# Kernel optimization log

Measured on AMD Instinct MI355X. Metric: run time of the kernel, lower is better.

Reference implementation:

```python
import jax, jax.numpy as jnp
import numpy as np
import math

B, S, D, H, L, DF = 16, 512, 512, 8, 6, 2048
DK = D // H
EPS = 1e-6


def _xavier(key, shape):
    # xavier_uniform over the last two dims (matches nn.init.xavier_uniform_)
    fan_in, fan_out = shape[-2], shape[-1]
    lim = math.sqrt(6.0 / (fan_in + fan_out))
    return jax.random.uniform(key, shape, jnp.float32, -lim, lim)


def setup_inputs() -> dict:
    key = jax.random.key(0)
    ks = jax.random.split(key, 12)
    return {
        "x": jax.random.normal(ks[0], (B, S, D), jnp.float32),
        "pe_table": jax.random.normal(ks[1], (S, D), jnp.float32),  # _4by8_pe weight
        "pe_q_w": _xavier(ks[2], (D, D)), "pe_q_b": jnp.zeros((D,), jnp.float32),
        "pe_k_w": _xavier(ks[3], (D, D)), "pe_k_b": jnp.zeros((D,), jnp.float32),
        "Wq": _xavier(ks[4], (L, D, D)), "bq": jnp.zeros((L, D), jnp.float32),
        "Wk": _xavier(ks[5], (L, D, D)), "bk": jnp.zeros((L, D), jnp.float32),
        "Wv": _xavier(ks[6], (L, D, D)), "bv": jnp.zeros((L, D), jnp.float32),
        "Wo": _xavier(ks[7], (L, D, D)), "bo": jnp.zeros((L, D), jnp.float32),
        "ln1_g": jnp.ones((L, D), jnp.float32), "ln1_b": jnp.zeros((L, D), jnp.float32),
        "W1": _xavier(ks[8], (L, D, DF)), "b1": jnp.zeros((L, DF), jnp.float32),
        "W2": _xavier(ks[9], (L, DF, D)), "b2": jnp.zeros((L, D), jnp.float32),
        "ln2_g": jnp.ones((L, D), jnp.float32), "ln2_b": jnp.zeros((L, D), jnp.float32),
    }


def _layernorm(y, g, b):
    m = jnp.mean(y, axis=-1, keepdims=True)
    v = jnp.var(y, axis=-1, keepdims=True)  # biased, as torch LayerNorm
    return (y - m) * jax.lax.rsqrt(v + EPS) * g + b


def reference(x, pe_table, pe_q_w, pe_q_b, pe_k_w, pe_k_b,
              Wq, bq, Wk, bk, Wv, bv, Wo, bo,
              ln1_g, ln1_b, W1, b1, W2, b2, ln2_g, ln2_b):
    scale = math.sqrt(2 * DK)
    h = x * math.sqrt(D)

    # scores_pe is identical for every batch element (pe_onehot = arange repeated)
    pq = (pe_table @ pe_q_w + pe_q_b).reshape(S, H, DK).transpose(1, 0, 2)  # [H,S,dk]
    pk = (pe_table @ pe_k_w + pe_k_b).reshape(S, H, DK).transpose(1, 0, 2)  # [H,S,dk]
    scores_pe = jnp.einsum('hqd,hkd->hqk', pq, pk) / scale  # [H,S,S]

    def step(h, p):
        wq, bq_, wk, bk_, wv, bv_, wo, bo_, g1, gb1, w1, fb1, w2, fb2, g2, gb2 = p
        q = (h @ wq + bq_).reshape(B, S, H, DK).transpose(0, 2, 1, 3)  # [B,H,S,dk]
        k = (h @ wk + bk_).reshape(B, S, H, DK).transpose(0, 2, 1, 3)
        v = (h @ wv + bv_).reshape(B, S, H, DK).transpose(0, 2, 1, 3)
        scores = jnp.einsum('bhqd,bhkd->bhqk', q, k) / scale + scores_pe  # [B,H,S,S]
        attn = jax.nn.softmax(scores, axis=-1)
        o = jnp.einsum('bhqk,bhkd->bhqd', attn, v).transpose(0, 2, 1, 3).reshape(B, S, D)
        o = o @ wo + bo_
        h1 = _layernorm(o + h, g1, gb1)
        f = jax.nn.gelu(h1 @ w1 + fb1, approximate=False) @ w2 + fb2
        h2 = _layernorm(f + h1, g2, gb2)
        return h2, None

    params = (Wq, bq, Wk, bk, Wv, bv, Wo, bo, ln1_g, ln1_b, W1, b1, W2, b2, ln2_g, ln2_b)
    h, _ = jax.lax.scan(step, h, params)
    pe_out = jnp.broadcast_to(pe_table, (B, S, D))
    return h, pe_out
```

## Files before the change

### kernel.cpp

```cpp
#include <hip/hip_runtime.h>
#include <hip/hip_bf16.h>

typedef __hip_bfloat16 bf16;
typedef short bf16x8 __attribute__((ext_vector_type(8)));
typedef float f32x4 __attribute__((ext_vector_type(4)));

#define DEV static __device__ __forceinline__

DEV f32x4 fzero4(){ f32x4 z; z[0]=0.f; z[1]=0.f; z[2]=0.f; z[3]=0.f; return z; }

DEV void gl2lds16(const bf16* g, bf16* l){
  __builtin_amdgcn_global_load_lds(
    (const __attribute__((address_space(1))) void*)g,
    (__attribute__((address_space(3))) void*)l, 16, 0, 0);
}

enum { EP_F32=0, EP_BF16=1, EP_GELU=2, EP_HILO=3, EP_QKV=4 };

template<int EPI, int NMT>
__global__ __launch_bounds__(256) void gemm_bt(
    const bf16* A0, const bf16* A1, const bf16* A2,
    const bf16* B0, const bf16* B1, const bf16* B2,
    int npass, int lda, int ldb, int M, int N, int K,
    const float* __restrict__ bs0, const float* __restrict__ bs1, const float* __restrict__ bs2,
    float alpha, void* o0, void* o1, void* o2,
    int nn, int mchunk, int azs, int bzs, int ozs)
{
  constexpr int BM = NMT*32;
  __shared__ __align__(16) bf16 As[2][BM*32];
  __shared__ __align__(16) bf16 Bs[2][128*32];
  const int t = threadIdx.x;
  const int lane = t & 63;
  const int w = t >> 6;
  const int wr = w >> 1, wc = w & 1;
  const int bid = blockIdx.x;
  const int xcd = bid & 7;
  const int idx = bid >> 3;
  const int qm = idx / nn;
  const int mb = xcd*mchunk + qm;
  const int nb = idx - qm*nn;
  const int m0 = mb*BM, n0 = nb*128;
  const int l15 = lane & 15, l4 = lane >> 4;
  const int grow = (lane >> 2);
  const int gcol = (lane & 3) * 8;
  const int z = blockIdx.z;
  if (azs){ A0 += (size_t)z*azs; if(A1) A1 += (size_t)z*azs; if(A2) A2 += (size_t)z*azs; }
  if (bzs){ B0 += (size_t)z*bzs; if(B1) B1 += (size_t)z*bzs; if(B2) B2 += (size_t)z*bzs; }

  auto Aof = [&](int p){ return (p==0)?A0:((p==1)?A1:A2); };
  auto Bof = [&](int p){ return (p==0)?B0:((p==1)?B1:B2); };

  auto stageAB = [&](int cb, const bf16* Ag, const bf16* Bg, int k0){
    if constexpr (NMT==4){
      #pragma unroll
      for (int q=0;q<2;q++){
        int row = w*32 + q*16 + grow;
        gl2lds16(Ag + (size_t)(m0+row)*lda + k0 + gcol, As[cb] + (w*32+q*16)*32);
        gl2lds16(Bg + (size_t)(n0+row)*ldb + k0 + gcol, Bs[cb] + (w*32+q*16)*32);
      }
    } else {
      int rA = w*16 + grow;
      gl2lds16(Ag + (size_t)(m0+rA)*lda + k0 + gcol, As[cb] + w*16*32);
      #pragma unroll
      for (int sb=0;sb<2;sb++){
        int rB = (2*w+sb)*16 + grow;
        gl2lds16(Bg + (size_t)(n0+rB)*ldb + k0 + gcol, Bs[cb] + (2*w+sb)*16*32);
      }
    }
  };

  f32x4 acc[NMT][4];
  #pragma unroll
  for (int i=0;i<NMT;i++)
    #pragma unroll
    for (int j=0;j<4;j++) acc[i][j] = fzero4();

  int cur = 0;
  stageAB(0, A0, B0, 0);
  for (int p=0;p<npass;p++){
    for (int k0=0;k0<K;k0+=32){
      __syncthreads();
      int kn = k0 + 32;
      if (kn < K)            stageAB(cur^1, Aof(p), Bof(p), kn);
      else if (p+1 < npass)  stageAB(cur^1, Aof(p+1), Bof(p+1), 0);
      bf16x8 af[NMT], bfv[4];
      #pragma unroll
      for (int mt=0;mt<NMT;mt++) af[mt] = *(const bf16x8*)(As[cur] + (wr*(NMT*16)+mt*16+l15)*32 + 8*l4);
      #pragma unroll
      for (int nt=0;nt<4;nt++) bfv[nt] = *(const bf16x8*)(Bs[cur] + (wc*64+nt*16+l15)*32 + 8*l4);
      #pragma unroll
      for (int mt=0;mt<NMT;mt++)
        #pragma unroll
        for (int nt=0;nt<4;nt++)
          acc[mt][nt] = __builtin_amdgcn_mfma_f32_16x16x32_bf16(af[mt], bfv[nt], acc[mt][nt], 0, 0, 0);
      cur ^= 1;
    }
  }

  #pragma unroll
  for (int mt=0;mt<NMT;mt++){
    #pragma unroll
    for (int nt=0;nt<4;nt++){
      const int crow = m0 + wr*(NMT*16) + mt*16 + l4*4;
      const int ccol = n0 + wc*64 + nt*16 + l15;
      #pragma unroll
      for (int j=0;j<4;j++){
        float v = acc[mt][nt][j];
        int r = crow + j;
        if (EPI==EP_F32){
          float b = bs0 ? bs0[ccol] : 0.f;
          ((float*)o0)[(size_t)r*N + ccol] = alpha*v + b;
        } else if (EPI==EP_BF16){
          float b = bs0 ? bs0[ccol] : 0.f;
          ((bf16*)o0 + (size_t)z*ozs)[(size_t)r*N + ccol] = __float2bfloat16(alpha*v + b);
        } else if (EPI==EP_GELU){
          float xx = v + bs0[ccol];
          float g = 0.5f*xx*(1.f + erff(xx*0.70710678118654752f));
          ((bf16*)o0)[(size_t)r*N + ccol] = __float2bfloat16(g);
        } else if (EPI==EP_HILO){
          float xx = v + bs0[ccol];
          bf16 hi = __float2bfloat16(xx);
          ((bf16*)o0)[(size_t)r*N + ccol] = hi;
          ((bf16*)o1)[(size_t)r*N + ccol] = __float2bfloat16(xx - __bfloat162float(hi));
        } else {
          int n = ccol;
          if (n < 512){
            ((bf16*)o0)[(size_t)r*512 + n] = __float2bfloat16(v + bs0[n]);
          } else if (n < 1024){
            ((bf16*)o1)[(size_t)r*512 + (n-512)] = __float2bfloat16(v + bs1[n-512]);
          } else {
            int d = n - 1024;
            int bb = r >> 9, s = r & 511;
            int hh = d >> 6, dd = d & 63;
            ((bf16*)o2)[(size_t)(((bb*8)+hh)*64 + dd)*512 + s] = __float2bfloat16(v + bs2[d]);
          }
        }
      }
    }
  }
}

template<int SPLIT>
__global__ __launch_bounds__(256) void attn_mfma(
  const bf16* __restrict__ Q, const bf16* __restrict__ Qlo,
  const bf16* __restrict__ Kh, const bf16* __restrict__ Klo,
  const bf16* __restrict__ VT, const bf16* __restrict__ SPE,
  bf16* __restrict__ O)
{
  __shared__ __align__(16) bf16 K_lds[64*64];
  __shared__ __align__(16) bf16 V_lds[64*64];
  __shared__ __align__(16) bf16 Klo_lds[SPLIT ? 64*64 : 8];
  __shared__ __align__(16) bf16 P_lds[4][16*64];
  const int t = threadIdx.x;
  const int lane = t & 63, w = t >> 6;
  const int l15 = lane & 15, l4 = lane >> 4;
  const int bid = blockIdx.x;
  const int h = bid & 7;
  const int s2 = bid >> 3;
  const int b = s2 >> 3, qblk = s2 & 7;
  const int q0 = qblk*64 + w*16;
  const float inv_scale = 0.08838834764831845f;
  const int xorv = (l15 & 7) << 3;

  bf16x8 qf[2], qflo[2];
  #pragma unroll
  for (int kst=0;kst<2;kst++){
    qf[kst] = *(const bf16x8*)(Q + (size_t)(b*512 + q0 + l15)*512 + h*64 + kst*32 + 8*l4);
    if (SPLIT) qflo[kst] = *(const bf16x8*)(Qlo + (size_t)(b*512 + q0 + l15)*512 + h*64 + kst*32 + 8*l4);
  }
  f32x4 accO[4];
  #pragma unroll
  for (int dt=0;dt<4;dt++) accO[dt] = fzero4();
  float mrow[4], lrow[4];
  #pragma unroll
  for (int j=0;j<4;j++){ mrow[j] = -1e30f; lrow[j] = 0.f; }

  const bf16* spe_h = SPE + (size_t)h*262144;
  const bf16* vbase = VT + (size_t)((b*8)+h)*32768;

  for (int n0=0;n0<512;n0+=64){
    #pragma unroll
    for (int st=0;st<2;st++){
      int rl = w*16 + st*8 + (lane>>3);
      int jj = (lane&7) ^ (rl&7);
      gl2lds16(Kh + (size_t)(b*512 + n0 + rl)*512 + h*64 + jj*8, K_lds + (w*16+st*8)*64);
      if (SPLIT)
        gl2lds16(Klo + (size_t)(b*512 + n0 + rl)*512 + h*64 + jj*8, Klo_lds + (w*16+st*8)*64);
      gl2lds16(vbase + (size_t)rl*512 + n0 + jj*8, V_lds + (w*16+st*8)*64);
    }
    __syncthreads();

    f32x4 sc[4];
    #pragma unroll
    for (int c=0;c<4;c++) sc[c] = fzero4();
    __builtin_amdgcn_s_setprio(1);
    #pragma unroll
    for (int c=0;c<4;c++){
      const int rr = c*16 + l15;
      #pragma unroll
      for (int kst=0;kst<2;kst++){
        bf16x8 kf = *(const bf16x8*)(K_lds + rr*64 + ((kst*32 + 8*l4) ^ xorv));
        sc[c] = __builtin_amdgcn_mfma_f32_16x16x32_bf16(qf[kst], kf, sc[c], 0,0,0);
        if (SPLIT){
          sc[c] = __builtin_amdgcn_mfma_f32_16x16x32_bf16(qflo[kst], kf, sc[c], 0,0,0);
          bf16x8 kfl = *(const bf16x8*)(Klo_lds + rr*64 + ((kst*32 + 8*l4) ^ xorv));
          sc[c] = __builtin_amdgcn_mfma_f32_16x16x32_bf16(qf[kst], kfl, sc[c], 0,0,0);
        }
      }
    }
    __builtin_amdgcn_s_setprio(0);
    float sv[4][4];
    #pragma unroll
    for (int c=0;c<4;c++)
      #pragma unroll
      for (int j=0;j<4;j++){
        int qr = q0 + l4*4 + j;
        sv[c][j] = sc[c][j]*inv_scale + __bfloat162float(spe_h[(size_t)qr*512 + n0 + c*16 + l15]);
      }
    float mx[4];
    float dm = -1e30f;
    #pragma unroll
    for (int j=0;j<4;j++){
      mx[j] = fmaxf(fmaxf(sv[0][j],sv[1][j]), fmaxf(sv[2][j],sv[3][j]));
      dm = fmaxf(dm, mx[j] - mrow[j]);
    }
    if (__any(dm > 8.f)){
      #pragma unroll
      for (int j=0;j<4;j++){
        float m2 = mx[j];
        m2 = fmaxf(m2, __shfl_xor(m2,1));
        m2 = fmaxf(m2, __shfl_xor(m2,2));
        m2 = fmaxf(m2, __shfl_xor(m2,4));
        m2 = fmaxf(m2, __shfl_xor(m2,8));
        float mn = fmaxf(mrow[j], m2);
        float fac = __expf(mrow[j] - mn);
        mrow[j] = mn;
        lrow[j] *= fac;
        #pragma unroll
        for (int dt=0;dt<4;dt++) accO[dt][j] *= fac;
      }
    }
    #pragma unroll
    for (int j=0;j<4;j++){
      int row = l4*4 + j;
      float ts = 0.f;
      #pragma unroll
      for (int c=0;c<4;c++){
        float pv = __expf(sv[c][j] - mrow[j]);
        ts += pv;
        P_lds[w][row*64 + ((c*16 + l15) ^ ((row&7)<<3))] = __float2bfloat16(pv);
      }
      ts += __shfl_xor(ts,1); ts += __shfl_xor(ts,2);
      ts += __shfl_xor(ts,4); ts += __shfl_xor(ts,8);
      lrow[j] += ts;
    }
    __builtin_amdgcn_s_setprio(1);
    #pragma unroll
    for (int kv=0;kv<2;kv++){
      bf16x8 pf = *(const bf16x8*)(P_lds[w] + l15*64 + ((kv*32 + 8*l4) ^ xorv));
      #pragma unroll
      for (int dt=0;dt<4;dt++){
        const int d = dt*16 + l15;
        bf16x8 vf = *(const bf16x8*)(V_lds + d*64 + ((kv*32 + 8*l4) ^ xorv));
        accO[dt] = __builtin_amdgcn_mfma_f32_16x16x32_bf16(pf, vf, accO[dt], 0,0,0);
      }
    }
    __builtin_amdgcn_s_setprio(0);
    __syncthreads();
  }
  #pragma unroll
  for (int dt=0;dt<4;dt++)
    #pragma unroll
    for (int j=0;j<4;j++){
      float v = accO[dt][j] / lrow[j];
      int r = q0 + l4*4 + j;
      O[(size_t)(b*512+r)*512 + h*64 + dt*16 + l15] = __float2bfloat16(v);
    }
}

__global__ __launch_bounds__(256) void ln_kernel(
  const float* __restrict__ tmp, const float* __restrict__ resid,
  const float* __restrict__ g, const float* __restrict__ bta,
  float* __restrict__ outf, bf16* __restrict__ outb)
{
  const int row = blockIdx.x*4 + (threadIdx.x>>6);
  const int lane = threadIdx.x & 63;
  const size_t base = (size_t)row*512 + lane*8;
  float4 a0 = *(const float4*)(tmp+base),   a1 = *(const float4*)(tmp+base+4);
  float4 r0 = *(const float4*)(resid+base), r1 = *(const float4*)(resid+base+4);
  float x[8];
  x[0]=a0.x+r0.x; x[1]=a0.y+r0.y; x[2]=a0.z+r0.z; x[3]=a0.w+r0.w;
  x[4]=a1.x+r1.x; x[5]=a1.y+r1.y; x[6]=a1.z+r1.z; x[7]=a1.w+r1.w;
  float s=0.f, sq=0.f;
  #pragma unroll
  for (int i=0;i<8;i++){ s += x[i]; sq += x[i]*x[i]; }
  #pragma unroll
  for (int d=1; d<64; d<<=1){ s += __shfl_xor(s,d); sq += __shfl_xor(sq,d); }
  float mean = s*(1.f/512.f);
  float var = sq*(1.f/512.f) - mean*mean;
  float rr = rsqrtf(var + 1e-6f);
  #pragma unroll
  for (int i=0;i<8;i++){
    int d = lane*8 + i;
    float y = (x[i]-mean)*rr*g[d] + bta[d];
    outf[base+i] = y;
    outb[base+i] = __float2bfloat16(y);
  }
}

template<bool LO>
__global__ __launch_bounds__(256) void tcast(
  const float* __restrict__ src, int srcStride,
  bf16* __restrict__ dst, int dstStride, bf16* __restrict__ dlo,
  int R, int C)
{
  __shared__ float tile[32][33];
  const int z = blockIdx.z;
  src += (size_t)z*srcStride;
  dst += (size_t)z*dstStride;
  const int tx = threadIdx.x & 31, ty = threadIdx.x >> 5;
  const int r0 = blockIdx.y*32, c0 = blockIdx.x*32;
  #pragma unroll
  for (int p=0;p<4;p++)
    tile[ty+8*p][tx] = src[(size_t)(r0+ty+8*p)*C + c0+tx];
  __syncthreads();
  #pragma unroll
  for (int p=0;p<4;p++){
    float v = tile[tx][ty+8*p];
    bf16 hi = __float2bfloat16(v);
    dst[(size_t)(c0+ty+8*p)*R + r0+tx] = hi;
    if (LO) dlo[(size_t)(c0+ty+8*p)*R + r0+tx] = __float2bfloat16(v - __bfloat162float(hi));
  }
}

__global__ void castbf(const float* __restrict__ in, bf16* __restrict__ out, int n){
  int i = blockIdx.x*blockDim.x + threadIdx.x;
  if (i < n) out[i] = __float2bfloat16(in[i]);
}

__global__ void init_h(const float* __restrict__ x, float* __restrict__ hf,
                       bf16* __restrict__ hb, bf16* __restrict__ hlo, int n){
  int i = blockIdx.x*blockDim.x + threadIdx.x;
  if (i < n){
    float v = x[i]*22.627416997969522f;
    hf[i] = v;
    bf16 hi = __float2bfloat16(v);
    hb[i] = hi;
    hlo[i] = __float2bfloat16(v - __bfloat162float(hi));
  }
}

__global__ void write_out(const float* __restrict__ hf, const float* __restrict__ pe,
                          float* __restrict__ out, int n1){
  int i = blockIdx.x*blockDim.x + threadIdx.x;
  if (i < n1){
    out[i] = hf[i];
    out[n1 + i] = pe[i & 262143];
  }
}

extern "C" void kernel_launch(void* const* d_in, const int* in_sizes, int n_in,
                              void* d_out, int out_size, void* d_ws, size_t ws_size,
                              hipStream_t stream)
{
  const float* x    = (const float*)d_in[0];
  const float* pe   = (const float*)d_in[1];
  const float* peqw = (const float*)d_in[2];
  const float* peqb = (const float*)d_in[3];
  const float* pekw = (const float*)d_in[4];
  const float* pekb = (const float*)d_in[5];
  const float* Wq   = (const float*)d_in[6];
  const float* bq   = (const float*)d_in[7];
  const float* Wk   = (const float*)d_in[8];
  const float* bk   = (const float*)d_in[9];
  const float* Wv   = (const float*)d_in[10];
  const float* bv   = (const float*)d_in[11];
  const float* Wo   = (const float*)d_in[12];
  const float* bo   = (const float*)d_in[13];
  const float* g1   = (const float*)d_in[14];
  const float* bb1  = (const float*)d_in[15];
  const float* W1   = (const float*)d_in[16];
  const float* fb1  = (const float*)d_in[17];
  const float* W2   = (const float*)d_in[18];
  const float* fb2  = (const float*)d_in[19];
  const float* g2   = (const float*)d_in[20];
  const float* bb2  = (const float*)d_in[21];

  char* wp = (char*)d_ws;
  auto carve = [&](size_t bytes)->void*{ void* r = (void*)wp; wp += (bytes + 255) & ~(size_t)255; return r; };
  float* hf   = (float*)carve(16777216);
  float* h1f  = (float*)carve(16777216);
  char*  regB = (char*)carve(16777216);
  float* tmp  = (float*)regB;
  bf16*  qlo  = (bf16*)regB;
  bf16*  klo  = (bf16*)(regB + 8388608);
  bf16* hb    = (bf16*)carve(8388608);
  bf16* hlo   = (bf16*)carve(8388608);
  bf16* h1b   = (bf16*)carve(8388608);
  char* regA  = (char*)carve(33554432);
  bf16* gbuf  = (bf16*)regA;
  bf16* qb    = (bf16*)regA;
  bf16* kbuf  = (bf16*)(regA + 8388608);
  bf16* vT    = (bf16*)(regA + 16777216);
  bf16* obuf  = (bf16*)(regA + 25165824);
  bf16* WqkvT = (bf16*)carve(9437184);
  bf16* WoT   = (bf16*)carve(3145728);
  bf16* W1T   = (bf16*)carve(12582912);
  bf16* W2T   = (bf16*)carve(12582912);
  bf16* Wq0h  = (bf16*)carve(524288);
  bf16* Wq0l  = (bf16*)carve(524288);
  bf16* Wk0h  = (bf16*)carve(524288);
  bf16* Wk0l  = (bf16*)carve(524288);
  bf16* peb   = (bf16*)carve(524288);
  bf16* pqwT  = (bf16*)carve(524288);
  bf16* pkwT  = (bf16*)carve(524288);
  bf16* pqb   = (bf16*)carve(524288);
  bf16* pkb   = (bf16*)carve(524288);
  bf16* spe   = (bf16*)carve(4194304);

  dim3 B256(256);
  const float INV_SCALE = 0.08838834764831845f;

  tcast<false><<<dim3(16,16,6),B256,0,stream>>>(Wq, 262144, WqkvT,          786432, nullptr, 512, 512);
  tcast<false><<<dim3(16,16,6),B256,0,stream>>>(Wk, 262144, WqkvT + 262144, 786432, nullptr, 512, 512);
  tcast<false><<<dim3(16,16,6),B256,0,stream>>>(Wv, 262144, WqkvT + 524288, 786432, nullptr, 512, 512);
  tcast<false><<<dim3(16,16,6),B256,0,stream>>>(Wo, 262144, WoT, 262144, nullptr, 512, 512);
  tcast<false><<<dim3(64,16,6),B256,0,stream>>>(W1, 1048576, W1T, 1048576, nullptr, 512, 2048);
  tcast<false><<<dim3(16,64,6),B256,0,stream>>>(W2, 1048576, W2T, 1048576, nullptr, 2048, 512);
  tcast<false><<<dim3(16,16,1),B256,0,stream>>>(peqw, 262144, pqwT, 262144, nullptr, 512, 512);
  tcast<false><<<dim3(16,16,1),B256,0,stream>>>(pekw, 262144, pkwT, 262144, nullptr, 512, 512);
  tcast<true ><<<dim3(16,16,1),B256,0,stream>>>(Wq, 262144, Wq0h, 262144, Wq0l, 512, 512);
  tcast<true ><<<dim3(16,16,1),B256,0,stream>>>(Wk, 262144, Wk0h, 262144, Wk0l, 512, 512);
  castbf<<<1024,B256,0,stream>>>(pe, peb, 262144);
  init_h<<<16384,B256,0,stream>>>(x, hf, hb, hlo, 4194304);

  gemm_bt<EP_BF16,2><<<dim3(32),B256,0,stream>>>(peb,nullptr,nullptr, pqwT,nullptr,nullptr, 1, 512,512, 512,512,512, peqb,nullptr,nullptr, 1.f, pqb,nullptr,nullptr, 4,1, 0,0,0);
  gemm_bt<EP_BF16,2><<<dim3(32),B256,0,stream>>>(peb,nullptr,nullptr, pkwT,nullptr,nullptr, 1, 512,512, 512,512,512, pekb,nullptr,nullptr, 1.f, pkb,nullptr,nullptr, 4,1, 0,0,0);
  gemm_bt<EP_BF16,2><<<dim3(32,1,8),B256,0,stream>>>(pqb,nullptr,nullptr, pkb,nullptr,nullptr, 1, 512,512, 512,512,64, nullptr,nullptr,nullptr, INV_SCALE, spe,nullptr,nullptr, 4,1, 64,64,262144);

  for (int l=0;l<6;l++){
    const bf16* WQKV = WqkvT + l*786432;
    const float* bql = bq + l*512;
    const float* bkl = bk + l*512;
    const float* bvl = bv + l*512;
    gemm_bt<EP_QKV,4><<<dim3(768),B256,0,stream>>>(hb,nullptr,nullptr, WQKV,nullptr,nullptr, 1, 512,512, 8192,1536,512, bql,bkl,bvl, 1.f, qb, kbuf, vT, 12,8, 0,0,0);
    if (l==0){
      gemm_bt<EP_HILO,2><<<dim3(512),B256,0,stream>>>(hb,hb,hlo, Wq0h,Wq0l,Wq0h, 3, 512,512, 8192,512,512, bql,nullptr,nullptr, 1.f, qb, qlo, nullptr, 4,16, 0,0,0);
      gemm_bt<EP_HILO,2><<<dim3(512),B256,0,stream>>>(hb,hb,hlo, Wk0h,Wk0l,Wk0h, 3, 512,512, 8192,512,512, bkl,nullptr,nullptr, 1.f, kbuf, klo, nullptr, 4,16, 0,0,0);
      attn_mfma<1><<<dim3(1024),B256,0,stream>>>(qb,qlo,kbuf,klo,vT,spe,obuf);
    } else {
      attn_mfma<0><<<dim3(1024),B256,0,stream>>>(qb,qb,kbuf,kbuf,vT,spe,obuf);
    }
    gemm_bt<EP_F32,2><<<dim3(512),B256,0,stream>>>(obuf,nullptr,nullptr, WoT+l*262144,nullptr,nullptr, 1, 512,512, 8192,512,512, bo+l*512,nullptr,nullptr, 1.f, tmp,nullptr,nullptr, 4,16, 0,0,0);
    ln_kernel<<<2048,B256,0,stream>>>(tmp, hf, g1+l*512, bb1+l*512, h1f, h1b);
    gemm_bt<EP_GELU,4><<<dim3(1024),B256,0,stream>>>(h1b,nullptr,nullptr, W1T+l*1048576,nullptr,nullptr, 1, 512,512, 8192,2048,512, fb1+l*2048,nullptr,nullptr, 1.f, gbuf,nullptr,nullptr, 16,8, 0,0,0);
    gemm_bt<EP_F32,2><<<dim3(512),B256,0,stream>>>(gbuf,nullptr,nullptr, W2T+l*1048576,nullptr,nullptr, 1, 2048,2048, 8192,512,2048, fb2+l*512,nullptr,nullptr, 1.f, tmp,nullptr,nullptr, 4,16, 0,0,0);
    ln_kernel<<<2048,B256,0,stream>>>(tmp, h1f, g2+l*512, bb2+l*512, hf, hb);
  }
  write_out<<<16384,B256,0,stream>>>(hf, pe, (float*)d_out, 4194304);
}
```

Baseline: 1.304 ms.

## Double-buffer attention K/V, fold softmax scale into Q, bf16 GEMM-LN intermediates

The attention kernel now double-buffers K/V tiles in LDS (non-split path), so the next tile's global-to-LDS load overlaps the current tile's compute. It also preloads the positional score bias as the MFMA accumulator init. The softmax scale and log2(e) are folded into Q and the PE scores so exp2f replaces __expf and the per-element scale multiply goes away. The rescale threshold is loosened from 8 to 12. The Wo and W2 GEMM outputs feeding LayerNorm are stored as bf16 instead of f32, halving that traffic at some accuracy cost, and a bit-shift bf16-to-float helper is added.

```diff
diff --git a/kernel.cpp b/kernel.cpp
--- a/kernel.cpp
+++ b/kernel.cpp
@@ -8,6 +8,15 @@
 #define DEV static __device__ __forceinline__
 
 DEV f32x4 fzero4(){ f32x4 z; z[0]=0.f; z[1]=0.f; z[2]=0.f; z[3]=0.f; return z; }
+
+DEV float bf2f(bf16 v){
+  unsigned int u = ((unsigned int)*(unsigned short*)&v) << 16;
+  return *(float*)&u;
+}
+DEV float bf2s(short s){
+  unsigned int u = ((unsigned int)(unsigned short)s) << 16;
+  return *(float*)&u;
+}
 
 DEV void gl2lds16(const bf16* g, bf16* l){
   __builtin_amdgcn_global_load_lds(
@@ -118,14 +127,14 @@
           float g = 0.5f*xx*(1.f + erff(xx*0.70710678118654752f));
           ((bf16*)o0)[(size_t)r*N + ccol] = __float2bfloat16(g);
         } else if (EPI==EP_HILO){
-          float xx = v + bs0[ccol];
+          float xx = (v + bs0[ccol]) * alpha;
           bf16 hi = __float2bfloat16(xx);
           ((bf16*)o0)[(size_t)r*N + ccol] = hi;
-          ((bf16*)o1)[(size_t)r*N + ccol] = __float2bfloat16(xx - __bfloat162float(hi));
+          ((bf16*)o1)[(size_t)r*N + ccol] = __float2bfloat16(xx - bf2f(hi));
         } else {
           int n = ccol;
           if (n < 512){
-            ((bf16*)o0)[(size_t)r*512 + n] = __float2bfloat16(v + bs0[n]);
+            ((bf16*)o0)[(size_t)r*512 + n] = __float2bfloat16((v + bs0[n]) * alpha);
           } else if (n < 1024){
             ((bf16*)o1)[(size_t)r*512 + (n-512)] = __float2bfloat16(v + bs1[n-512]);
           } else {
@@ -147,8 +156,9 @@
   const bf16* __restrict__ VT, const bf16* __restrict__ SPE,
   bf16* __restrict__ O)
 {
-  __shared__ __align__(16) bf16 K_lds[64*64];
-  __shared__ __align__(16) bf16 V_lds[64*64];
+  constexpr int NB = SPLIT ? 1 : 2;
+  __shared__ __align__(16) bf16 K_lds[NB][64*64];
+  __shared__ __align__(16) bf16 V_lds[NB][64*64];
   __shared__ __align__(16) bf16 Klo_lds[SPLIT ? 64*64 : 8];
   __shared__ __align__(16) bf16 P_lds[4][16*64];
   const int t = threadIdx.x;
@@ -159,8 +169,22 @@
   const int s2 = bid >> 3;
   const int b = s2 >> 3, qblk = s2 & 7;
   const int q0 = qblk*64 + w*16;
-  const float inv_scale = 0.08838834764831845f;
   const int xorv = (l15 & 7) << 3;
+
+  const bf16* spe_h = SPE + (size_t)h*262144;
+  const bf16* vbase = VT + (size_t)((b*8)+h)*32768;
+
+  auto stageKV = [&](int cb, int n0){
+    #pragma unroll
+    for (int st=0;st<2;st++){
+      int rl = w*16 + st*8 + (lane>>3);
+      int jj = (lane&7) ^ (rl&7);
+      gl2lds16(Kh + (size_t)(b*512 + n0 + rl)*512 + h*64 + jj*8, K_lds[cb] + (w*16+st*8)*64);
+      if (SPLIT)
+        gl2lds16(Klo + (size_t)(b*512 + n0 + rl)*512 + h*64 + jj*8, Klo_lds + (w*16+st*8)*64);
+      gl2lds16(vbase + (size_t)rl*512 + n0 + jj*8, V_lds[cb] + (w*16+st*8)*64);
+    }
+  };
 
   bf16x8 qf[2], qflo[2];
   #pragma unroll
@@ -175,31 +199,24 @@
   #pragma unroll
   for (int j=0;j<4;j++){ mrow[j] = -1e30f; lrow[j] = 0.f; }
 
-  const bf16* spe_h = SPE + (size_t)h*262144;
-  const bf16* vbase = VT + (size_t)((b*8)+h)*32768;
-
-  for (int n0=0;n0<512;n0+=64){
-    #pragma unroll
-    for (int st=0;st<2;st++){
-      int rl = w*16 + st*8 + (lane>>3);
-      int jj = (lane&7) ^ (rl&7);
-      gl2lds16(Kh + (size_t)(b*512 + n0 + rl)*512 + h*64 + jj*8, K_lds + (w*16+st*8)*64);
-      if (SPLIT)
-        gl2lds16(Klo + (size_t)(b*512 + n0 + rl)*512 + h*64 + jj*8, Klo_lds + (w*16+st*8)*64);
-      gl2lds16(vbase + (size_t)rl*512 + n0 + jj*8, V_lds + (w*16+st*8)*64);
-    }
+  int cur = 0;
+  stageKV(0, 0);
+  for (int it=0; it<8; ++it){
+    const int n0 = it*64;
+    f32x4 sc[4];
+    #pragma unroll
+    for (int c=0;c<4;c++)
+      #pragma unroll
+      for (int j=0;j<4;j++)
+        sc[c][j] = bf2f(spe_h[(size_t)(q0 + l4*4 + j)*512 + n0 + c*16 + l15]);
     __syncthreads();
-
-    f32x4 sc[4];
-    #pragma unroll
-    for (int c=0;c<4;c++) sc[c] = fzero4();
-    __builtin_amdgcn_s_setprio(1);
+    if (NB==2 && it+1 < 8) stageKV(cur^1, n0+64);
     #pragma unroll
     for (int c=0;c<4;c++){
       const int rr = c*16 + l15;
       #pragma unroll
       for (int kst=0;kst<2;kst++){
-        bf16x8 kf = *(const bf16x8*)(K_lds + rr*64 + ((kst*32 + 8*l4) ^ xorv));
+        bf16x8 kf = *(const bf16x8*)(K_lds[cur] + rr*64 + ((kst*32 + 8*l4) ^ xorv));
         sc[c] = __builtin_amdgcn_mfma_f32_16x16x32_bf16(qf[kst], kf, sc[c], 0,0,0);
         if (SPLIT){
           sc[c] = __builtin_amdgcn_mfma_f32_16x16x32_bf16(qflo[kst], kf, sc[c], 0,0,0);
@@ -208,23 +225,14 @@
         }
       }
     }
-    __builtin_amdgcn_s_setprio(0);
-    float sv[4][4];
-    #pragma unroll
-    for (int c=0;c<4;c++)
-      #pragma unroll
-      for (int j=0;j<4;j++){
-        int qr = q0 + l4*4 + j;
-        sv[c][j] = sc[c][j]*inv_scale + __bfloat162float(spe_h[(size_t)qr*512 + n0 + c*16 + l15]);
-      }
     float mx[4];
     float dm = -1e30f;
     #pragma unroll
     for (int j=0;j<4;j++){
-      mx[j] = fmaxf(fmaxf(sv[0][j],sv[1][j]), fmaxf(sv[2][j],sv[3][j]));
+      mx[j] = fmaxf(fmaxf(sc[0][j],sc[1][j]), fmaxf(sc[2][j],sc[3][j]));
       dm = fmaxf(dm, mx[j] - mrow[j]);
     }
-    if (__any(dm > 8.f)){
+    if (__any(dm > 12.f)){
       #pragma unroll
       for (int j=0;j<4;j++){
         float m2 = mx[j];
@@ -233,7 +241,7 @@
         m2 = fmaxf(m2, __shfl_xor(m2,4));
         m2 = fmaxf(m2, __shfl_xor(m2,8));
         float mn = fmaxf(mrow[j], m2);
-        float fac = __expf(mrow[j] - mn);
+        float fac = exp2f(mrow[j] - mn);
         mrow[j] = mn;
         lrow[j] *= fac;
         #pragma unroll
@@ -246,7 +254,7 @@
       float ts = 0.f;
       #pragma unroll
       for (int c=0;c<4;c++){
-        float pv = __expf(sv[c][j] - mrow[j]);
+        float pv = exp2f(sc[c][j] - mrow[j]);
         ts += pv;
         P_lds[w][row*64 + ((c*16 + l15) ^ ((row&7)<<3))] = __float2bfloat16(pv);
       }
@@ -254,19 +262,21 @@
       ts += __shfl_xor(ts,4); ts += __shfl_xor(ts,8);
       lrow[j] += ts;
     }
-    __builtin_amdgcn_s_setprio(1);
     #pragma unroll
     for (int kv=0;kv<2;kv++){
       bf16x8 pf = *(const bf16x8*)(P_lds[w] + l15*64 + ((kv*32 + 8*l4) ^ xorv));
       #pragma unroll
       for (int dt=0;dt<4;dt++){
         const int d = dt*16 + l15;
-        bf16x8 vf = *(const bf16x8*)(V_lds + d*64 + ((kv*32 + 8*l4) ^ xorv));
+        bf16x8 vf = *(const bf16x8*)(V_lds[cur] + d*64 + ((kv*32 + 8*l4) ^ xorv));
         accO[dt] = __builtin_amdgcn_mfma_f32_16x16x32_bf16(pf, vf, accO[dt], 0,0,0);
       }
     }
-    __builtin_amdgcn_s_setprio(0);
-    __syncthreads();
+    if (NB==1){
+      __syncthreads();
+      if (it+1 < 8) stageKV(0, n0+64);
+    }
+    cur ^= (NB-1);
   }
   #pragma unroll
   for (int dt=0;dt<4;dt++)
@@ -279,18 +289,20 @@
 }
 
 __global__ __launch_bounds__(256) void ln_kernel(
-  const float* __restrict__ tmp, const float* __restrict__ resid,
+  const bf16* __restrict__ tmp, const float* __restrict__ resid,
   const float* __restrict__ g, const float* __restrict__ bta,
   float* __restrict__ outf, bf16* __restrict__ outb)
 {
   const int row = blockIdx.x*4 + (threadIdx.x>>6);
   const int lane = threadIdx.x & 63;
   const size_t base = (size_t)row*512 + lane*8;
-  float4 a0 = *(const float4*)(tmp+base),   a1 = *(const float4*)(tmp+base+4);
+  bf16x8 a = *(const bf16x8*)(tmp+base);
   float4 r0 = *(const float4*)(resid+base), r1 = *(const float4*)(resid+base+4);
   float x[8];
-  x[0]=a0.x+r0.x; x[1]=a0.y+r0.y; x[2]=a0.z+r0.z; x[3]=a0.w+r0.w;
-  x[4]=a1.x+r1.x; x[5]=a1.y+r1.y; x[6]=a1.z+r1.z; x[7]=a1.w+r1.w;
+  x[0]=bf2s(a[0])+r0.x; x[1]=bf2s(a[1])+r0.y;
+  x[2]=bf2s(a[2])+r0.z; x[3]=bf2s(a[3])+r0.w;
+  x[4]=bf2s(a[4])+r1.x; x[5]=bf2s(a[5])+r1.y;
+  x[6]=bf2s(a[6])+r1.z; x[7]=bf2s(a[7])+r1.w;
   float s=0.f, sq=0.f;
   #pragma unroll
   for (int i=0;i<8;i++){ s += x[i]; sq += x[i]*x[i]; }
@@ -329,7 +341,7 @@
     float v = tile[tx][ty+8*p];
     bf16 hi = __float2bfloat16(v);
     dst[(size_t)(c0+ty+8*p)*R + r0+tx] = hi;
-    if (LO) dlo[(size_t)(c0+ty+8*p)*R + r0+tx] = __float2bfloat16(v - __bfloat162float(hi));
+    if (LO) dlo[(size_t)(c0+ty+8*p)*R + r0+tx] = __float2bfloat16(v - bf2f(hi));
   }
 }
 
@@ -346,7 +358,7 @@
     hf[i] = v;
     bf16 hi = __float2bfloat16(v);
     hb[i] = hi;
-    hlo[i] = __float2bfloat16(v - __bfloat162float(hi));
+    hlo[i] = __float2bfloat16(v - bf2f(hi));
   }
 }
 
@@ -391,7 +403,7 @@
   float* hf   = (float*)carve(16777216);
   float* h1f  = (float*)carve(16777216);
   char*  regB = (char*)carve(16777216);
-  float* tmp  = (float*)regB;
+  bf16*  tmpb = (bf16*)regB;
   bf16*  qlo  = (bf16*)regB;
   bf16*  klo  = (bf16*)(regB + 8388608);
   bf16* hb    = (bf16*)carve(8388608);
@@ -419,7 +431,7 @@
   bf16* spe   = (bf16*)carve(4194304);
 
   dim3 B256(256);
-  const float INV_SCALE = 0.08838834764831845f;
+  const float QSCALE = 0.08838834764831845f * 1.4426950408889634f;
 
   tcast<false><<<dim3(16,16,6),B256,0,stream>>>(Wq, 262144, WqkvT,          786432, nullptr, 512, 512);
   tcast<false><<<dim3(16,16,6),B256,0,stream>>>(Wk, 262144, WqkvT + 262144, 786432, nullptr, 512, 512);
@@ -436,26 +448,26 @@
 
   gemm_bt<EP_BF16,2><<<dim3(32),B256,0,stream>>>(peb,nullptr,nullptr, pqwT,nullptr,nullptr, 1, 512,512, 512,512,512, peqb,nullptr,nullptr, 1.f, pqb,nullptr,nullptr, 4,1, 0,0,0);
   gemm_bt<EP_BF16,2><<<dim3(32),B256,0,stream>>>(peb,nullptr,nullptr, pkwT,nullptr,nullptr, 1, 512,512, 512,512,512, pekb,nullptr,nullptr, 1.f, pkb,nullptr,nullptr, 4,1, 0,0,0);
-  gemm_bt<EP_BF16,2><<<dim3(32,1,8),B256,0,stream>>>(pqb,nullptr,nullptr, pkb,nullptr,nullptr, 1, 512,512, 512,512,64, nullptr,nullptr,nullptr, INV_SCALE, spe,nullptr,nullptr, 4,1, 64,64,262144);
+  gemm_bt<EP_BF16,2><<<dim3(32,1,8),B256,0,stream>>>(pqb,nullptr,nullptr, pkb,nullptr,nullptr, 1, 512,512, 512,512,64, nullptr,nullptr,nullptr, QSCALE, spe,nullptr,nullptr, 4,1, 64,64,262144);
 
   for (int l=0;l<6;l++){
     const bf16* WQKV = WqkvT + l*786432;
     const float* bql = bq + l*512;
     const float* bkl = bk + l*512;
     const float* bvl = bv + l*512;
-    gemm_bt<EP_QKV,4><<<dim3(768),B256,0,stream>>>(hb,nullptr,nullptr, WQKV,nullptr,nullptr, 1, 512,512, 8192,1536,512, bql,bkl,bvl, 1.f, qb, kbuf, vT, 12,8, 0,0,0);
+    gemm_bt<EP_QKV,4><<<dim3(768),B256,0,stream>>>(hb,nullptr,nullptr, WQKV,nullptr,nullptr, 1, 512,512, 8192,1536,512, bql,bkl,bvl, QSCALE, qb, kbuf, vT, 12,8, 0,0,0);
     if (l==0){
-      gemm_bt<EP_HILO,2><<<dim3(512),B256,0,stream>>>(hb,hb,hlo, Wq0h,Wq0l,Wq0h, 3, 512,512, 8192,512,512, bql,nullptr,nullptr, 1.f, qb, qlo, nullptr, 4,16, 0,0,0);
+      gemm_bt<EP_HILO,2><<<dim3(512),B256,0,stream>>>(hb,hb,hlo, Wq0h,Wq0l,Wq0h, 3, 512,512, 8192,512,512, bql,nullptr,nullptr, QSCALE, qb, qlo, nullptr, 4,16, 0,0,0);
       gemm_bt<EP_HILO,2><<<dim3(512),B256,0,stream>>>(hb,hb,hlo, Wk0h,Wk0l,Wk0h, 3, 512,512, 8192,512,512, bkl,nullptr,nullptr, 1.f, kbuf, klo, nullptr, 4,16, 0,0,0);
       attn_mfma<1><<<dim3(1024),B256,0,stream>>>(qb,qlo,kbuf,klo,vT,spe,obuf);
     } else {
       attn_mfma<0><<<dim3(1024),B256,0,stream>>>(qb,qb,kbuf,kbuf,vT,spe,obuf);
     }
-    gemm_bt<EP_F32,2><<<dim3(512),B256,0,stream>>>(obuf,nullptr,nullptr, WoT+l*262144,nullptr,nullptr, 1, 512,512, 8192,512,512, bo+l*512,nullptr,nullptr, 1.f, tmp,nullptr,nullptr, 4,16, 0,0,0);
-    ln_kernel<<<2048,B256,0,stream>>>(tmp, hf, g1+l*512, bb1+l*512, h1f, h1b);
+    gemm_bt<EP_BF16,2><<<dim3(512),B256,0,stream>>>(obuf,nullptr,nullptr, WoT+l*262144,nullptr,nullptr, 1, 512,512, 8192,512,512, bo+l*512,nullptr,nullptr, 1.f, tmpb,nullptr,nullptr, 4,16, 0,0,0);
+    ln_kernel<<<2048,B256,0,stream>>>(tmpb, hf, g1+l*512, bb1+l*512, h1f, h1b);
     gemm_bt<EP_GELU,4><<<dim3(1024),B256,0,stream>>>(h1b,nullptr,nullptr, W1T+l*1048576,nullptr,nullptr, 1, 512,512, 8192,2048,512, fb1+l*2048,nullptr,nullptr, 1.f, gbuf,nullptr,nullptr, 16,8, 0,0,0);
-    gemm_bt<EP_F32,2><<<dim3(512),B256,0,stream>>>(gbuf,nullptr,nullptr, W2T+l*1048576,nullptr,nullptr, 1, 2048,2048, 8192,512,2048, fb2+l*512,nullptr,nullptr, 1.f, tmp,nullptr,nullptr, 4,16, 0,0,0);
-    ln_kernel<<<2048,B256,0,stream>>>(tmp, h1f, g2+l*512, bb2+l*512, hf, hb);
+    gemm_bt<EP_BF16,2><<<dim3(512),B256,0,stream>>>(gbuf,nullptr,nullptr, W2T+l*1048576,nullptr,nullptr, 1, 2048,2048, 8192,512,2048, fb2+l*512,nullptr,nullptr, 1.f, tmpb,nullptr,nullptr, 4,16, 0,0,0);
+    ln_kernel<<<2048,B256,0,stream>>>(tmpb, h1f, g2+l*512, bb2+l*512, hf, hb);
   }
   write_out<<<16384,B256,0,stream>>>(hf, pe, (float*)d_out, 4194304);
 }
```

New measurement: 1.295 ms. Within noise of the previous version (-0.7%).
